# Performance work log

Measured on AMD Instinct MI355X. Metric: run time of the kernel, lower is better.

The kernel has to match this reference:

```python
import jax, jax.numpy as jnp
import numpy as np

N = 100000
IN_C = 128
HID = 128
LAT = 64
E = 800000


def gcn_conv(x, src, dst, norm, W, b, num_nodes):
    # x: [N, Cin]; src/dst: [E+N] (self-loops appended); norm: [E+N]
    xw = x @ W                                   # [N, Cout]
    msg = xw[src] * norm[:, None]                # gather + scale, [E+N, Cout]
    out = jax.ops.segment_sum(msg, dst, num_segments=num_nodes)
    return out + b


def setup_inputs() -> dict:
    key = jax.random.key(0)
    ks = jax.random.split(key, 8)
    x = jax.random.normal(ks[0], (N, IN_C), dtype=jnp.float32)
    edge_index = jax.random.randint(ks[1], (2, E), 0, N, dtype=jnp.int64)
    batch = jnp.zeros((N,), dtype=jnp.int64)
    # GCNConv params (Glorot-ish scale)
    W1 = jax.random.normal(ks[2], (IN_C, HID), dtype=jnp.float32) / np.sqrt(IN_C)
    b1 = jnp.zeros((HID,), dtype=jnp.float32)
    Wmu = jax.random.normal(ks[3], (HID, LAT), dtype=jnp.float32) / np.sqrt(HID)
    bmu = jnp.zeros((LAT,), dtype=jnp.float32)
    Wlv = jax.random.normal(ks[4], (HID, LAT), dtype=jnp.float32) / np.sqrt(HID)
    blv = jnp.zeros((LAT,), dtype=jnp.float32)
    return {"x": x, "edge_index": edge_index, "batch": batch,
            "W1": W1, "b1": b1, "Wmu": Wmu, "bmu": bmu, "Wlv": Wlv, "blv": blv}


def reference(x, edge_index, batch, W1, b1, Wmu, bmu, Wlv, blv):
    num_nodes = x.shape[0]
    loop = jnp.arange(num_nodes, dtype=edge_index.dtype)
    src = jnp.concatenate([edge_index[0], loop])   # source nodes (+self loops)
    dst = jnp.concatenate([edge_index[1], loop])   # target nodes (+self loops)
    # symmetric GCN normalization: deg over targets, norm = d[src]^-1/2 * d[dst]^-1/2
    deg = jax.ops.segment_sum(jnp.ones_like(dst, dtype=x.dtype), dst,
                              num_segments=num_nodes)
    dis = jnp.where(deg > 0, jax.lax.rsqrt(deg), 0.0)
    norm = dis[src] * dis[dst]                      # [E+N]

    h = jax.nn.relu(gcn_conv(x, src, dst, norm, W1, b1, num_nodes))
    mu = gcn_conv(h, src, dst, norm, Wmu, bmu, num_nodes)
    logvar = gcn_conv(h, src, dst, norm, Wlv, blv, num_nodes)
    return (mu, logvar)
```

## Files before the change

kernel.cpp:

```cpp
#include <hip/hip_runtime.h>

typedef short bf16x8 __attribute__((ext_vector_type(8)));
typedef float f32x4 __attribute__((ext_vector_type(4)));

#define ELLK 32
#define OCAP 4096
#define CSTRIDE 16

static __device__ __forceinline__ float4 f4zero() { return make_float4(0.f, 0.f, 0.f, 0.f); }

static __device__ __forceinline__ unsigned short f2bf(float f) {
  unsigned u = __float_as_uint(f);
  u += 0x7FFFu + ((u >> 16) & 1u);
  return (unsigned short)(u >> 16);
}
static __device__ __forceinline__ float2 bf2x2(unsigned u) {
  float2 r;
  r.x = __uint_as_float(u << 16);
  r.y = __uint_as_float(u & 0xFFFF0000u);
  return r;
}

__global__ void k_setup(const float* __restrict__ W1, const float* __restrict__ Wmu,
                        const float* __restrict__ Wlv, unsigned short* __restrict__ Wt1,
                        unsigned short* __restrict__ Wt2, uint4* __restrict__ cntz,
                        int* __restrict__ ocount, int nz4, int nbz) {
  int b = blockIdx.x;
  if (b < nbz) {
    int i = b * 256 + threadIdx.x;
    if (i < nz4) cntz[i] = make_uint4(0u, 0u, 0u, 0u);
    if (b == 0 && threadIdx.x == 0) *ocount = 0;
  } else {
    int id = (b - nbz) * 256 + threadIdx.x;
    if (id < 16384) {
      int nn = id >> 7, k = id & 127;
      Wt1[id] = f2bf(W1[k * 128 + nn]);
    } else {
      int id2 = id - 16384;
      int nn = id2 >> 7, k = id2 & 127;
      float v = (nn < 64) ? Wmu[k * 64 + nn] : Wlv[k * 64 + (nn - 64)];
      Wt2[id2] = f2bf(v);
    }
  }
}

__global__ void k_fill(const int* __restrict__ ei, int* __restrict__ cnt,
                       int* __restrict__ ell, int2* __restrict__ ovf,
                       int* __restrict__ ocount, int E) {
  int e = blockIdx.x * 256 + threadIdx.x;
  if (e >= E) return;
  int s = ei[e];
  int d = ei[E + e];
  int pos = atomicAdd(&cnt[(size_t)d * CSTRIDE], 1);
  if (pos < ELLK) {
    ell[(size_t)d * ELLK + pos] = s;
  } else {
    int o = atomicAdd(ocount, 1);
    if (o < OCAP) ovf[o] = make_int2(d, s);
  }
}

__global__ void k_dnorm(const int* __restrict__ cnt, float* __restrict__ dnorm,
                        unsigned* __restrict__ mflag, int n) {
  int i = blockIdx.x * 256 + threadIdx.x;
  if (i >= n) return;
  int c = cnt[(size_t)i * CSTRIDE];
  dnorm[i] = rsqrtf((float)(c + 1));
  int m = (c < ELLK) ? c : ELLK;
  mflag[i] = (unsigned)m | ((c > ELLK) ? 0x80000000u : 0u);
}

__global__ __launch_bounds__(256) void k_gemm1(
    const float* __restrict__ x, const unsigned short* __restrict__ Wt,
    const float* __restrict__ dnorm, unsigned short* __restrict__ A, int n) {
  __shared__ unsigned short Wl[128 * 136];
  __shared__ unsigned short Xl[64 * 136];
  const int tid = threadIdx.x;
  const int row0 = blockIdx.x * 64;
  {
    const uint4* Wg = (const uint4*)Wt;
#pragma unroll
    for (int i = 0; i < 8; ++i) {
      int idx = tid + i * 256;
      int r = idx >> 4, c = idx & 15;
      *(uint4*)&Wl[r * 136 + c * 8] = Wg[r * 16 + c];
    }
  }
  {
#pragma unroll
    for (int i = 0; i < 8; ++i) {
      int idx = tid + i * 256;
      int r = idx >> 5, c = idx & 31;
      int gi = row0 + r;
      float4 v = (gi < n) ? ((const float4*)x)[(size_t)gi * 32 + c] : f4zero();
      ushort4 p;
      p.x = f2bf(v.x); p.y = f2bf(v.y); p.z = f2bf(v.z); p.w = f2bf(v.w);
      *(ushort4*)&Xl[r * 136 + c * 4] = p;
    }
  }
  __syncthreads();

  const int wave = tid >> 6, lane = tid & 63;
  const int li = lane & 15, quad = lane >> 4;
  const int m0 = wave * 16;
  f32x4 acc[8];
#pragma unroll
  for (int t = 0; t < 8; ++t) acc[t] = (f32x4){0.f, 0.f, 0.f, 0.f};

#pragma unroll
  for (int kk = 0; kk < 4; ++kk) {
    int ko = kk * 32 + quad * 8;
    bf16x8 a = *(const bf16x8*)&Xl[(m0 + li) * 136 + ko];
#pragma unroll
    for (int nt = 0; nt < 8; ++nt) {
      bf16x8 b = *(const bf16x8*)&Wl[(nt * 16 + li) * 136 + ko];
      acc[nt] = __builtin_amdgcn_mfma_f32_16x16x32_bf16(a, b, acc[nt], 0, 0, 0);
    }
  }
  float dn[4];
#pragma unroll
  for (int r = 0; r < 4; ++r) {
    int gi = row0 + m0 + quad * 4 + r;
    dn[r] = (gi < n) ? dnorm[gi] : 0.f;
  }
  __syncthreads();
#pragma unroll
  for (int nt = 0; nt < 8; ++nt)
#pragma unroll
    for (int r = 0; r < 4; ++r)
      Xl[(m0 + quad * 4 + r) * 136 + nt * 16 + li] = f2bf(acc[nt][r] * dn[r]);
  __syncthreads();
  {
    uint4* A4 = (uint4*)A;
#pragma unroll
    for (int i = 0; i < 4; ++i) {
      int idx = tid + i * 256;
      int r = idx >> 4, c = idx & 15;
      int gi = row0 + r;
      if (gi < n) A4[(size_t)gi * 16 + c] = *(uint4*)&Xl[r * 136 + c * 8];
    }
  }
}

template <bool EPI_RELU>
__global__ __launch_bounds__(256) void k_spmm(
    const unsigned* __restrict__ mflag, const float* __restrict__ dnorm,
    const int* __restrict__ ell, const int2* __restrict__ ovf,
    const int* __restrict__ ocount, const unsigned* __restrict__ S,
    unsigned* __restrict__ D, const float2* __restrict__ bias, int n) {
  int wid = (blockIdx.x * blockDim.x + threadIdx.x) >> 6;
  if (wid >= n) return;
  int lane = threadIdx.x & 63;

  unsigned mf = mflag[wid];
  int m = (int)(mf & 0xFFFFu);
  float dsd = dnorm[wid];
  float2 acc = bf2x2(S[(size_t)wid * 64 + lane]);

  const int* row = ell + (size_t)wid * ELLK;
  int j = 0;
  for (; j + 3 < m; j += 4) {
    int4 ss = *(const int4*)(row + j);
    float2 u0 = bf2x2(S[(size_t)ss.x * 64 + lane]);
    float2 u1 = bf2x2(S[(size_t)ss.y * 64 + lane]);
    float2 u2 = bf2x2(S[(size_t)ss.z * 64 + lane]);
    float2 u3 = bf2x2(S[(size_t)ss.w * 64 + lane]);
    acc.x += u0.x + u1.x + u2.x + u3.x;
    acc.y += u0.y + u1.y + u2.y + u3.y;
  }
  for (; j < m; ++j) {
    int s = row[j];
    float2 u0 = bf2x2(S[(size_t)s * 64 + lane]);
    acc.x += u0.x;
    acc.y += u0.y;
  }
  if (mf & 0x80000000u) {
    int oc = *ocount;
    if (oc > OCAP) oc = OCAP;
    for (int k = 0; k < oc; ++k) {
      int2 e = ovf[k];
      if (e.x == wid) {
        float2 u0 = bf2x2(S[(size_t)e.y * 64 + lane]);
        acc.x += u0.x;
        acc.y += u0.y;
      }
    }
  }
  float2 o;
  if (EPI_RELU) {
    float2 b = bias[lane];
    o.x = dsd * fmaxf(fmaf(dsd, acc.x, b.x), 0.f);
    o.y = dsd * fmaxf(fmaf(dsd, acc.y, b.y), 0.f);
  } else {
    o.x = dsd * acc.x;
    o.y = dsd * acc.y;
  }
  unsigned pk = (unsigned)f2bf(o.x) | ((unsigned)f2bf(o.y) << 16);
  D[(size_t)wid * 64 + lane] = pk;
}

__global__ __launch_bounds__(256) void k_gemm2_mfma(
    const unsigned short* __restrict__ G, const unsigned short* __restrict__ Wt,
    const float* __restrict__ bmu, const float* __restrict__ blv,
    float* __restrict__ out, int n) {
  __shared__ unsigned short Wl[128 * 136];
  __shared__ unsigned short Xl[64 * 136];
  const int tid = threadIdx.x;
  const int row0 = blockIdx.x * 64;
  {
    const uint4* Wg = (const uint4*)Wt;
#pragma unroll
    for (int i = 0; i < 8; ++i) {
      int idx = tid + i * 256;
      int r = idx >> 4, c = idx & 15;
      *(uint4*)&Wl[r * 136 + c * 8] = Wg[r * 16 + c];
    }
  }
  {
    const uint4* Gg = (const uint4*)G;
#pragma unroll
    for (int i = 0; i < 4; ++i) {
      int idx = tid + i * 256;
      int r = idx >> 4, c = idx & 15;
      int gi = row0 + r;
      uint4 v = (gi < n) ? Gg[(size_t)gi * 16 + c] : make_uint4(0, 0, 0, 0);
      *(uint4*)&Xl[r * 136 + c * 8] = v;
    }
  }
  __syncthreads();

  const int wave = tid >> 6, lane = tid & 63;
  const int li = lane & 15, quad = lane >> 4;
  const int m0 = wave * 16;

  float bias[8];
#pragma unroll
  for (int nt = 0; nt < 8; ++nt) {
    int c = nt * 16 + li;
    bias[nt] = (c < 64) ? bmu[c] : blv[c - 64];
  }

  f32x4 acc[8];
#pragma unroll
  for (int t = 0; t < 8; ++t) acc[t] = (f32x4){0.f, 0.f, 0.f, 0.f};

#pragma unroll
  for (int kk = 0; kk < 4; ++kk) {
    int ko = kk * 32 + quad * 8;
    bf16x8 a = *(const bf16x8*)&Xl[(m0 + li) * 136 + ko];
#pragma unroll
    for (int nt = 0; nt < 8; ++nt) {
      bf16x8 b = *(const bf16x8*)&Wl[(nt * 16 + li) * 136 + ko];
      acc[nt] = __builtin_amdgcn_mfma_f32_16x16x32_bf16(a, b, acc[nt], 0, 0, 0);
    }
  }
#pragma unroll
  for (int nt = 0; nt < 8; ++nt) {
    int col = nt * 16 + li;
#pragma unroll
    for (int r = 0; r < 4; ++r) {
      int gi = row0 + m0 + quad * 4 + r;
      if (gi < n) {
        float v = acc[nt][r] + bias[nt];
        if (col < 64) out[(size_t)gi * 64 + col] = v;
        else          out[(size_t)(n + gi) * 64 + (col - 64)] = v;
      }
    }
  }
}

extern "C" void kernel_launch(void* const* d_in, const int* in_sizes, int n_in,
                              void* d_out, int out_size, void* d_ws, size_t ws_size,
                              hipStream_t stream) {
  const float* x   = (const float*)d_in[0];
  const int*   ei  = (const int*)d_in[1];
  const float* W1  = (const float*)d_in[3];
  const float* b1  = (const float*)d_in[4];
  const float* Wmu = (const float*)d_in[5];
  const float* bmu = (const float*)d_in[6];
  const float* Wlv = (const float*)d_in[7];
  const float* blv = (const float*)d_in[8];
  float* out = (float*)d_out;

  const int n = in_sizes[0] / 128;
  const int E = in_sizes[1] / 2;

  float* ws = (float*)d_ws;
  size_t p = 0;
  int* cnt    = (int*)(ws + p); p += (size_t)n * CSTRIDE;
  int* ocount = (int*)(ws + p); p += 1;
  p = (p + 3) & ~(size_t)3;
  int* ell    = (int*)(ws + p); p += (size_t)n * ELLK;
  int2* ovf   = (int2*)(ws + p); p += (size_t)OCAP * 2;
  unsigned* A = (unsigned*)(ws + p); p += (size_t)n * 64;
  unsigned* H = (unsigned*)(ws + p); p += (size_t)n * 64;
  unsigned* G = (unsigned*)(ws + p); p += (size_t)n * 64;
  unsigned short* Wt1 = (unsigned short*)(ws + p); p += 8192;
  unsigned short* Wt2 = (unsigned short*)(ws + p); p += 8192;
  float* dnorm    = (float*)(ws + p); p += n;
  unsigned* mflag = (unsigned*)(ws + p); p += n;

  int nz4  = (n * CSTRIDE) / 4;
  int nbz  = (nz4 + 255) / 256;
  int eb   = (E + 255) / 256;
  int gblk = (n + 63) / 64;
  int nb   = (n + 255) / 256;
  int sblk = (n + 3) / 4;

  k_setup<<<nbz + 128, 256, 0, stream>>>(W1, Wmu, Wlv, Wt1, Wt2, (uint4*)cnt, ocount, nz4, nbz);
  k_fill<<<eb, 256, 0, stream>>>(ei, cnt, ell, ovf, ocount, E);
  k_dnorm<<<nb, 256, 0, stream>>>(cnt, dnorm, mflag, n);
  k_gemm1<<<gblk, 256, 0, stream>>>(x, Wt1, dnorm, (unsigned short*)A, n);
  k_spmm<true><<<sblk, 256, 0, stream>>>(mflag, dnorm, ell, ovf, ocount, A, H,
                                         (const float2*)b1, n);
  k_spmm<false><<<sblk, 256, 0, stream>>>(mflag, dnorm, ell, ovf, ocount, H, G, nullptr, n);
  k_gemm2_mfma<<<gblk, 256, 0, stream>>>((const unsigned short*)G, Wt2, bmu, blv, out, n);
}
```

Measured before the change: 300.2 us.

## Transpose ELL to column-major and batch gathers by 8 with zero-row padding

Stores the ELL neighbor table in slot-major order and rewrites the spmm loop to issue eight index loads and eight feature gathers per batch. Out-of-range slots are redirected to an appended zero row in A and H, so there is no tail loop. The aim is more outstanding memory requests per wave. In exchange, each index load is a separate strided access instead of one vector load per four entries, and padded slots do wasted gathers.

```diff
diff --git a/kernel.cpp b/kernel.cpp
--- a/kernel.cpp
+++ b/kernel.cpp
@@ -46,14 +46,14 @@
 
 __global__ void k_fill(const int* __restrict__ ei, int* __restrict__ cnt,
                        int* __restrict__ ell, int2* __restrict__ ovf,
-                       int* __restrict__ ocount, int E) {
+                       int* __restrict__ ocount, int E, int n) {
   int e = blockIdx.x * 256 + threadIdx.x;
   if (e >= E) return;
   int s = ei[e];
   int d = ei[E + e];
   int pos = atomicAdd(&cnt[(size_t)d * CSTRIDE], 1);
   if (pos < ELLK) {
-    ell[(size_t)d * ELLK + pos] = s;
+    ell[(size_t)pos * n + d] = s;
   } else {
     int o = atomicAdd(ocount, 1);
     if (o < OCAP) ovf[o] = make_int2(d, s);
@@ -61,7 +61,13 @@
 }
 
 __global__ void k_dnorm(const int* __restrict__ cnt, float* __restrict__ dnorm,
-                        unsigned* __restrict__ mflag, int n) {
+                        unsigned* __restrict__ mflag, unsigned* __restrict__ A,
+                        unsigned* __restrict__ H, int n) {
+  if (blockIdx.x == 0 && threadIdx.x < 128) {
+    int t = threadIdx.x;
+    if (t < 64) A[(size_t)n * 64 + t] = 0u;
+    else        H[(size_t)n * 64 + (t - 64)] = 0u;
+  }
   int i = blockIdx.x * 256 + threadIdx.x;
   if (i >= n) return;
   int c = cnt[(size_t)i * CSTRIDE];
@@ -157,22 +163,24 @@
   float dsd = dnorm[wid];
   float2 acc = bf2x2(S[(size_t)wid * 64 + lane]);
 
-  const int* row = ell + (size_t)wid * ELLK;
-  int j = 0;
-  for (; j + 3 < m; j += 4) {
-    int4 ss = *(const int4*)(row + j);
-    float2 u0 = bf2x2(S[(size_t)ss.x * 64 + lane]);
-    float2 u1 = bf2x2(S[(size_t)ss.y * 64 + lane]);
-    float2 u2 = bf2x2(S[(size_t)ss.z * 64 + lane]);
-    float2 u3 = bf2x2(S[(size_t)ss.w * 64 + lane]);
-    acc.x += u0.x + u1.x + u2.x + u3.x;
-    acc.y += u0.y + u1.y + u2.y + u3.y;
-  }
-  for (; j < m; ++j) {
-    int s = row[j];
-    float2 u0 = bf2x2(S[(size_t)s * 64 + lane]);
-    acc.x += u0.x;
-    acc.y += u0.y;
+  const int* ep = ell + wid;
+  int nbt = (m + 7) >> 3;
+  for (int b = 0; b < nbt; ++b) {
+    int j0 = b * 8;
+    int idx[8];
+#pragma unroll
+    for (int k = 0; k < 8; ++k) idx[k] = ep[(size_t)(j0 + k) * n];
+#pragma unroll
+    for (int k = 0; k < 8; ++k) idx[k] = (j0 + k < m) ? idx[k] : n;
+    unsigned u[8];
+#pragma unroll
+    for (int k = 0; k < 8; ++k) u[k] = S[(size_t)idx[k] * 64 + lane];
+#pragma unroll
+    for (int k = 0; k < 8; ++k) {
+      float2 f = bf2x2(u[k]);
+      acc.x += f.x;
+      acc.y += f.y;
+    }
   }
   if (mf & 0x80000000u) {
     int oc = *ocount;
@@ -292,8 +300,8 @@
   p = (p + 3) & ~(size_t)3;
   int* ell    = (int*)(ws + p); p += (size_t)n * ELLK;
   int2* ovf   = (int2*)(ws + p); p += (size_t)OCAP * 2;
-  unsigned* A = (unsigned*)(ws + p); p += (size_t)n * 64;
-  unsigned* H = (unsigned*)(ws + p); p += (size_t)n * 64;
+  unsigned* A = (unsigned*)(ws + p); p += (size_t)(n + 1) * 64;
+  unsigned* H = (unsigned*)(ws + p); p += (size_t)(n + 1) * 64;
   unsigned* G = (unsigned*)(ws + p); p += (size_t)n * 64;
   unsigned short* Wt1 = (unsigned short*)(ws + p); p += 8192;
   unsigned short* Wt2 = (unsigned short*)(ws + p); p += 8192;
@@ -308,8 +316,8 @@
   int sblk = (n + 3) / 4;
 
   k_setup<<<nbz + 128, 256, 0, stream>>>(W1, Wmu, Wlv, Wt1, Wt2, (uint4*)cnt, ocount, nz4, nbz);
-  k_fill<<<eb, 256, 0, stream>>>(ei, cnt, ell, ovf, ocount, E);
-  k_dnorm<<<nb, 256, 0, stream>>>(cnt, dnorm, mflag, n);
+  k_fill<<<eb, 256, 0, stream>>>(ei, cnt, ell, ovf, ocount, E, n);
+  k_dnorm<<<nb, 256, 0, stream>>>(cnt, dnorm, mflag, A, H, n);
   k_gemm1<<<gblk, 256, 0, stream>>>(x, Wt1, dnorm, (unsigned short*)A, n);
   k_spmm<true><<<sblk, 256, 0, stream>>>(mflag, dnorm, ell, ovf, ocount, A, H,
                                          (const float2*)b1, n);
```

Result: no change. 298.7 us (-0.5%).
